# Optimization experiments

Hardware: AMD Instinct MI355X
Metric: run time of the kernel (lower is better)

Reference implementation:

```python
import jax, jax.numpy as jnp
import numpy as np

N_NODES = 100000
N_EDGES = 1200000
IN_DIM = 64
HID = 64
N_GRAPHS = 512
N_CLASSES = 1
LN_EPS = 1e-5
NORM_EPS = 1e-12


def _layer_norm(x, g, b):
    mu = x.mean(-1, keepdims=True)
    var = ((x - mu) ** 2).mean(-1, keepdims=True)
    return (x - mu) * jax.lax.rsqrt(var + LN_EPS) * g + b


def setup_inputs() -> dict:
    key = jax.random.key(0)
    ks = jax.random.split(key, 20)
    h = jax.random.normal(ks[0], (N_NODES, IN_DIM), jnp.float32)
    src = jax.random.randint(ks[1], (N_EDGES,), 0, N_NODES)
    dst = jax.random.randint(ks[2], (N_EDGES,), 0, N_NODES)
    graph_ids = jnp.sort(jax.random.randint(ks[3], (N_NODES,), 0, N_GRAPHS))
    s1 = 1.0 / np.sqrt(IN_DIM)
    s2 = 1.0 / np.sqrt(HID)
    s3 = 1.0 / np.sqrt(2 * HID)
    return {
        "h": h, "src": src, "dst": dst, "graph_ids": graph_ids,
        "W1": jax.random.normal(ks[4], (IN_DIM, HID), jnp.float32) * s1,
        "b1": jnp.zeros((HID,), jnp.float32),
        "W2": jax.random.normal(ks[5], (HID, HID), jnp.float32) * s2,
        "b2": jnp.zeros((HID,), jnp.float32),
        "g1": jnp.ones((HID,), jnp.float32), "be1": jnp.zeros((HID,), jnp.float32),
        "g2": jnp.ones((HID,), jnp.float32), "be2": jnp.zeros((HID,), jnp.float32),
        "g3": jnp.ones((HID,), jnp.float32), "be3": jnp.zeros((HID,), jnp.float32),
        "g4": jnp.ones((HID,), jnp.float32), "be4": jnp.zeros((HID,), jnp.float32),
        "Wc1": jax.random.normal(ks[6], (2 * HID, HID), jnp.float32) * s3,
        "bc1": jnp.zeros((HID,), jnp.float32),
        "Wc2": jax.random.normal(ks[7], (HID, HID), jnp.float32) * s2,
        "bc2": jnp.zeros((HID,), jnp.float32),
        "Wc3": jax.random.normal(ks[8], (HID, N_CLASSES), jnp.float32) * s2,
        "bc3": jnp.zeros((N_CLASSES,), jnp.float32),
    }


def reference(h, src, dst, graph_ids, W1, b1, W2, b2, g1, be1, g2, be2,
              g3, be3, g4, be4, Wc1, bc1, Wc2, bc2, Wc3, bc3):
    N = N_NODES
    ones_e = jnp.ones((src.shape[0],), jnp.float32)
    # DGL GraphConv norm='both': symmetric degree normalization (clamp 0 -> 1)
    deg_out = jnp.clip(jax.ops.segment_sum(ones_e, src, num_segments=N), 1.0)
    deg_in = jnp.clip(jax.ops.segment_sum(ones_e, dst, num_segments=N), 1.0)
    ns = (deg_out ** -0.5)[:, None]
    nd = (deg_in ** -0.5)[:, None]

    def conv(x, W, b):
        msg = (x * ns)[src]                                  # [E, d] gather
        agg = jax.ops.segment_sum(msg, dst, num_segments=N)  # [N, d] scatter-add
        return (agg * nd) @ W + b

    h1 = jax.nn.relu(_layer_norm(conv(h, W1, b1), g1, be1))
    h1 = jax.nn.relu(_layer_norm(conv(h1, W2, b2), g2, be2))

    # per-graph mean / max pooling (dgl.mean_nodes / dgl.max_nodes)
    ssum = jax.ops.segment_sum(h1, graph_ids, num_segments=N_GRAPHS)
    cnt = jnp.clip(jax.ops.segment_sum(jnp.ones((N,), jnp.float32), graph_ids,
                                       num_segments=N_GRAPHS), 1.0)
    hg = ssum / cnt[:, None]
    hg_max = jax.ops.segment_max(h1, graph_ids, num_segments=N_GRAPHS)

    def l2norm(x):  # F.normalize(p=2, dim=1)
        n = jnp.sqrt((x * x).sum(-1, keepdims=True))
        return x / jnp.maximum(n, NORM_EPS)

    hg = jnp.concatenate([l2norm(hg), l2norm(hg_max)], axis=1)  # [G, 2*HID]
    out = jax.nn.relu(_layer_norm(hg @ Wc1 + bc1, g3, be3))
    out = jax.nn.relu(_layer_norm(out @ Wc2 + bc2, g4, be4))
    return out @ Wc3 + bc3
```

## Files before the change

### kernel.cpp

```cpp
#include <hip/hip_runtime.h>
#include <math.h>

#define HID 64
#define LN_EPS 1e-5f
#define NORM_EPS 1e-12f
#define CHUNK 1024
#define CONV_BLOCKS 2048

__device__ __forceinline__ float wave_sum64(float v) {
#pragma unroll
    for (int o = 32; o > 0; o >>= 1) v += __shfl_xor(v, o, 64);
    return v;
}

__global__ __launch_bounds__(256) void count_kernel(const int* __restrict__ src,
                                                    const int* __restrict__ dst,
                                                    int* __restrict__ cnt_out,
                                                    int* __restrict__ cnt_in,
                                                    int E) {
    int e = blockIdx.x * 256 + threadIdx.x;
    if (e >= E) return;
    atomicAdd(&cnt_out[src[e]], 1);
    atomicAdd(&cnt_in[dst[e]], 1);
}

__global__ __launch_bounds__(256) void norm_kernel(int* __restrict__ cnt_out,
                                                   const int* __restrict__ cnt_in,
                                                   float* __restrict__ ns,
                                                   float* __restrict__ nd,
                                                   int N) {
    int n = blockIdx.x * 256 + threadIdx.x;
    if (n >= N) return;
    ns[n] = rsqrtf((float)max(cnt_out[n], 1));
    nd[n] = rsqrtf((float)max(cnt_in[n], 1));
    cnt_out[n] = 0;
}

__global__ __launch_bounds__(256) void scan1_kernel(const int* __restrict__ cnt,
                                                    int* __restrict__ cs,
                                                    int* __restrict__ partials,
                                                    int N) {
    __shared__ int wsum[4];
    int t = threadIdx.x;
    int lane = t & 63, wave = t >> 6;
    int base = blockIdx.x * CHUNK + t * 4;
    int v0 = (base + 0 < N) ? cnt[base + 0] : 0;
    int v1 = (base + 1 < N) ? cnt[base + 1] : 0;
    int v2 = (base + 2 < N) ? cnt[base + 2] : 0;
    int v3 = (base + 3 < N) ? cnt[base + 3] : 0;
    int tsum = v0 + v1 + v2 + v3;
    int x = tsum;
#pragma unroll
    for (int off = 1; off < 64; off <<= 1) {
        int y = __shfl_up(x, off, 64);
        if (lane >= off) x += y;
    }
    if (lane == 63) wsum[wave] = x;
    __syncthreads();
    int waveoff = 0;
    for (int w = 0; w < wave; ++w) waveoff += wsum[w];
    int off0 = waveoff + x - tsum;
    if (base + 0 < N) cs[base + 0] = off0;
    if (base + 1 < N) cs[base + 1] = off0 + v0;
    if (base + 2 < N) cs[base + 2] = off0 + v0 + v1;
    if (base + 3 < N) cs[base + 3] = off0 + v0 + v1 + v2;
    if (t == 255) partials[blockIdx.x] = waveoff + x;
}

__global__ __launch_bounds__(256) void scan2_kernel(int* __restrict__ partials, int nch) {
    __shared__ int wsum[4];
    int t = threadIdx.x;
    int lane = t & 63, wave = t >> 6;
    int base = t * 4;
    int v0 = (base + 0 < nch) ? partials[base + 0] : 0;
    int v1 = (base + 1 < nch) ? partials[base + 1] : 0;
    int v2 = (base + 2 < nch) ? partials[base + 2] : 0;
    int v3 = (base + 3 < nch) ? partials[base + 3] : 0;
    int tsum = v0 + v1 + v2 + v3;
    int x = tsum;
#pragma unroll
    for (int off = 1; off < 64; off <<= 1) {
        int y = __shfl_up(x, off, 64);
        if (lane >= off) x += y;
    }
    if (lane == 63) wsum[wave] = x;
    __syncthreads();
    int waveoff = 0;
    for (int w = 0; w < wave; ++w) waveoff += wsum[w];
    int off0 = waveoff + x - tsum;
    if (base + 0 < nch) partials[base + 0] = off0;
    if (base + 1 < nch) partials[base + 1] = off0 + v0;
    if (base + 2 < nch) partials[base + 2] = off0 + v0 + v1;
    if (base + 3 < nch) partials[base + 3] = off0 + v0 + v1 + v2;
}

__global__ __launch_bounds__(256) void scan3_kernel(int* __restrict__ cs,
                                                    const int* __restrict__ partials,
                                                    int N, int E) {
    int n = blockIdx.x * 256 + threadIdx.x;
    if (n < N) cs[n] += partials[n / CHUNK];
    if (n == 0) cs[N] = E;
}

__global__ __launch_bounds__(256) void fill_kernel(const int* __restrict__ src,
                                                   const int* __restrict__ dst,
                                                   const float* __restrict__ ns,
                                                   const int* __restrict__ cs,
                                                   int* __restrict__ cursor,
                                                   int2* __restrict__ epack,
                                                   int E) {
    int e = blockIdx.x * 256 + threadIdx.x;
    if (e >= E) return;
    int s = src[e];
    int d = dst[e];
    float w = ns[s];
    int p = cs[d] + atomicAdd(&cursor[d], 1);
    epack[p] = make_int2(s, __float_as_int(w));
}

__global__ __launch_bounds__(256) void conv_kernel(const float* __restrict__ x,
                                                   const int2* __restrict__ epack,
                                                   const int* __restrict__ cs,
                                                   const float* __restrict__ nd,
                                                   const float* __restrict__ W,
                                                   const float* __restrict__ b,
                                                   const float* __restrict__ gam,
                                                   const float* __restrict__ bet,
                                                   float* __restrict__ out,
                                                   int N) {
    __shared__ float Ws[HID * HID];
    int tid = threadIdx.x;
    for (int i = tid; i < HID * HID / 4; i += 256) {
        reinterpret_cast<float4*>(Ws)[i] = reinterpret_cast<const float4*>(W)[i];
    }
    __syncthreads();
    int wave = tid >> 6;
    int lane = tid & 63;
    float bl = b[lane], gl = gam[lane], bel = bet[lane];

    for (int n = blockIdx.x * 4 + wave; n < N; n += CONV_BLOCKS * 4) {
        int beg = cs[n], end = cs[n + 1];
        float acc = 0.0f;
        int e = beg;
        for (; e + 4 <= end; e += 4) {
            int2 p0 = epack[e + 0];
            int2 p1 = epack[e + 1];
            int2 p2 = epack[e + 2];
            int2 p3 = epack[e + 3];
            float v0 = x[(size_t)p0.x * HID + lane];
            float v1 = x[(size_t)p1.x * HID + lane];
            float v2 = x[(size_t)p2.x * HID + lane];
            float v3 = x[(size_t)p3.x * HID + lane];
            acc = fmaf(v0, __int_as_float(p0.y), acc);
            acc = fmaf(v1, __int_as_float(p1.y), acc);
            acc = fmaf(v2, __int_as_float(p2.y), acc);
            acc = fmaf(v3, __int_as_float(p3.y), acc);
        }
        for (; e < end; ++e) {
            int2 p = epack[e];
            acc = fmaf(x[(size_t)p.x * HID + lane], __int_as_float(p.y), acc);
        }
        float t = acc * nd[n];

        float y = bl;
#pragma unroll
        for (int k = 0; k < HID; ++k) {
            y = fmaf(__shfl(t, k, 64), Ws[k * HID + lane], y);
        }
        float mu = wave_sum64(y) * (1.0f / HID);
        float d = y - mu;
        float var = wave_sum64(d * d) * (1.0f / HID);
        float o = d * rsqrtf(var + LN_EPS) * gl + bel;
        o = fmaxf(o, 0.0f);
        out[(size_t)n * HID + lane] = o;
    }
}

__global__ __launch_bounds__(256) void pool_kernel(const float* __restrict__ h1,
                                                   const int* __restrict__ gid,
                                                   float* __restrict__ gsum,
                                                   int* __restrict__ gmax,
                                                   float* __restrict__ gcnt,
                                                   int N) {
    int wave = threadIdx.x >> 6;
    int lane = threadIdx.x & 63;
    int strip = blockIdx.x * 4 + wave;
    int base = strip * 64;
    if (base >= N) return;
    int nmax = min(64, N - base);
    int gv = (base + lane < N) ? gid[base + lane] : -1;
    int gcur = __shfl(gv, 0, 64);
    float sum = 0.0f, mx = 0.0f;
    int cnt = 0;
    for (int i = 0; i < nmax; ++i) {
        int g = __shfl(gv, i, 64);
        if (g != gcur) {
            atomicAdd(&gsum[(size_t)gcur * HID + lane], sum);
            atomicMax(&gmax[(size_t)gcur * HID + lane], __float_as_int(mx));
            if (lane == 0) atomicAdd(&gcnt[gcur], (float)cnt);
            sum = 0.0f; mx = 0.0f; cnt = 0; gcur = g;
        }
        float v = h1[((size_t)base + i) * HID + lane];
        sum += v;
        mx = fmaxf(mx, v);
        cnt++;
    }
    atomicAdd(&gsum[(size_t)gcur * HID + lane], sum);
    atomicMax(&gmax[(size_t)gcur * HID + lane], __float_as_int(mx));
    if (lane == 0) atomicAdd(&gcnt[gcur], (float)cnt);
}

__global__ __launch_bounds__(64) void head_kernel(const float* __restrict__ gsum,
                                                  const int* __restrict__ gmax,
                                                  const float* __restrict__ gcnt,
                                                  const float* __restrict__ Wc1,
                                                  const float* __restrict__ bc1,
                                                  const float* __restrict__ g3,
                                                  const float* __restrict__ be3,
                                                  const float* __restrict__ Wc2,
                                                  const float* __restrict__ bc2,
                                                  const float* __restrict__ g4,
                                                  const float* __restrict__ be4,
                                                  const float* __restrict__ Wc3,
                                                  const float* __restrict__ bc3,
                                                  float* __restrict__ out) {
    __shared__ float hg[2 * HID];
    __shared__ float t1[HID];
    int g = blockIdx.x;
    int lane = threadIdx.x;

    float cnt = fmaxf(gcnt[g], 1.0f);
    float mean = gsum[(size_t)g * HID + lane] / cnt;
    float mx = __int_as_float(gmax[(size_t)g * HID + lane]);

    float s1 = sqrtf(wave_sum64(mean * mean));
    float a = mean / fmaxf(s1, NORM_EPS);
    float s2 = sqrtf(wave_sum64(mx * mx));
    float bmx = mx / fmaxf(s2, NORM_EPS);

    hg[lane] = a;
    hg[HID + lane] = bmx;
    __syncthreads();

    float y = bc1[lane];
#pragma unroll 8
    for (int k = 0; k < 2 * HID; ++k) {
        y = fmaf(hg[k], Wc1[k * HID + lane], y);
    }
    float mu = wave_sum64(y) * (1.0f / HID);
    float d = y - mu;
    float var = wave_sum64(d * d) * (1.0f / HID);
    float o = d * rsqrtf(var + LN_EPS) * g3[lane] + be3[lane];
    o = fmaxf(o, 0.0f);
    t1[lane] = o;
    __syncthreads();

    float y2 = bc2[lane];
#pragma unroll 8
    for (int k = 0; k < HID; ++k) {
        y2 = fmaf(t1[k], Wc2[k * HID + lane], y2);
    }
    mu = wave_sum64(y2) * (1.0f / HID);
    d = y2 - mu;
    var = wave_sum64(d * d) * (1.0f / HID);
    o = d * rsqrtf(var + LN_EPS) * g4[lane] + be4[lane];
    o = fmaxf(o, 0.0f);

    float v = o * Wc3[lane];
    v = wave_sum64(v);
    if (lane == 0) out[g] = v + bc3[0];
}

extern "C" void kernel_launch(void* const* d_in, const int* in_sizes, int n_in,
                              void* d_out, int out_size, void* d_ws, size_t ws_size,
                              hipStream_t stream) {
    const float* h   = (const float*)d_in[0];
    const int*   src = (const int*)d_in[1];
    const int*   dst = (const int*)d_in[2];
    const int*   gid = (const int*)d_in[3];
    const float* W1  = (const float*)d_in[4];
    const float* b1  = (const float*)d_in[5];
    const float* W2  = (const float*)d_in[6];
    const float* b2  = (const float*)d_in[7];
    const float* g1  = (const float*)d_in[8];
    const float* be1 = (const float*)d_in[9];
    const float* g2  = (const float*)d_in[10];
    const float* be2 = (const float*)d_in[11];
    const float* g3  = (const float*)d_in[12];
    const float* be3 = (const float*)d_in[13];
    const float* g4  = (const float*)d_in[14];
    const float* be4 = (const float*)d_in[15];
    const float* Wc1 = (const float*)d_in[16];
    const float* bc1 = (const float*)d_in[17];
    const float* Wc2 = (const float*)d_in[18];
    const float* bc2 = (const float*)d_in[19];
    const float* Wc3 = (const float*)d_in[20];
    const float* bc3 = (const float*)d_in[21];
    float* out = (float*)d_out;

    const int N = in_sizes[0] / HID;
    const int E = in_sizes[1];
    const int G = out_size;

    char* ws = (char*)d_ws;
    float* h1     = (float*)ws;
    float* h2     = h1 + (size_t)N * HID;
    int2*  epack  = (int2*)(h2 + (size_t)N * HID);
    float* ns     = (float*)(epack + E);
    float* nd     = ns + N;
    int*   cnt_out= (int*)(nd + N);
    int*   cnt_in = cnt_out + N;
    int*   cs     = cnt_in + N;
    int*   partials = cs + N + 4;
    float* gsum   = (float*)(partials + 1024);
    int*   gmax   = (int*)(gsum + (size_t)G * HID);
    float* gcnt   = (float*)(gmax + (size_t)G * HID);

    const int nch = (N + CHUNK - 1) / CHUNK;

    hipMemsetAsync(cnt_out, 0, sizeof(int) * (size_t)2 * N, stream);
    hipMemsetAsync(gsum, 0, sizeof(float) * (size_t)G * (2 * HID + 1), stream);

    count_kernel<<<(E + 255) / 256, 256, 0, stream>>>(src, dst, cnt_out, cnt_in, E);
    norm_kernel<<<(N + 255) / 256, 256, 0, stream>>>(cnt_out, cnt_in, ns, nd, N);
    scan1_kernel<<<nch, 256, 0, stream>>>(cnt_in, cs, partials, N);
    scan2_kernel<<<1, 256, 0, stream>>>(partials, nch);
    scan3_kernel<<<(N + 255) / 256, 256, 0, stream>>>(cs, partials, N, E);
    fill_kernel<<<(E + 255) / 256, 256, 0, stream>>>(src, dst, ns, cs, cnt_out, epack, E);

    conv_kernel<<<CONV_BLOCKS, 256, 0, stream>>>(h, epack, cs, nd, W1, b1, g1, be1, h1, N);
    conv_kernel<<<CONV_BLOCKS, 256, 0, stream>>>(h1, epack, cs, nd, W2, b2, g2, be2, h2, N);

    int nstrips = (N + 63) / 64;
    pool_kernel<<<(nstrips + 3) / 4, 256, 0, stream>>>(h2, gid, gsum, gmax, gcnt, N);

    head_kernel<<<G, 64, 0, stream>>>(gsum, gmax, gcnt, Wc1, bc1, g3, be3,
                                      Wc2, bc2, g4, be4, Wc3, bc3, out);
}
```

Before: 539.4 us.

## Fuse degree norm into scan, vectorize edge kernels, segment-based pooling

Merges the degree-normalization kernel into the first scan pass and precomputes per-node cursors so the fill step skips reading row offsets. Count and fill kernels each process four edges per thread with vector loads. Pooling now assigns one block per graph, locating its node range by binary search on sorted graph ids, which removes atomics and a memset. The conv kernel gets an occupancy hint and a reduced unroll of the matvec loop, which may change register pressure.

```diff
diff --git a/kernel.cpp b/kernel.cpp
--- a/kernel.cpp
+++ b/kernel.cpp
@@ -13,30 +13,40 @@
     return v;
 }
 
+__device__ __forceinline__ int lower_bound_dev(const int* __restrict__ a, int n, int key) {
+    int lo = 0, hi = n;
+    while (lo < hi) {
+        int mid = (lo + hi) >> 1;
+        if (a[mid] < key) lo = mid + 1; else hi = mid;
+    }
+    return lo;
+}
+
 __global__ __launch_bounds__(256) void count_kernel(const int* __restrict__ src,
                                                     const int* __restrict__ dst,
                                                     int* __restrict__ cnt_out,
                                                     int* __restrict__ cnt_in,
                                                     int E) {
-    int e = blockIdx.x * 256 + threadIdx.x;
-    if (e >= E) return;
-    atomicAdd(&cnt_out[src[e]], 1);
-    atomicAdd(&cnt_in[dst[e]], 1);
-}
-
-__global__ __launch_bounds__(256) void norm_kernel(int* __restrict__ cnt_out,
-                                                   const int* __restrict__ cnt_in,
-                                                   float* __restrict__ ns,
-                                                   float* __restrict__ nd,
-                                                   int N) {
-    int n = blockIdx.x * 256 + threadIdx.x;
-    if (n >= N) return;
-    ns[n] = rsqrtf((float)max(cnt_out[n], 1));
-    nd[n] = rsqrtf((float)max(cnt_in[n], 1));
-    cnt_out[n] = 0;
-}
-
-__global__ __launch_bounds__(256) void scan1_kernel(const int* __restrict__ cnt,
+    int e0 = (blockIdx.x * 256 + threadIdx.x) * 4;
+    if (e0 + 3 < E) {
+        int4 s4 = *reinterpret_cast<const int4*>(src + e0);
+        int4 d4 = *reinterpret_cast<const int4*>(dst + e0);
+        atomicAdd(&cnt_out[s4.x], 1); atomicAdd(&cnt_out[s4.y], 1);
+        atomicAdd(&cnt_out[s4.z], 1); atomicAdd(&cnt_out[s4.w], 1);
+        atomicAdd(&cnt_in[d4.x], 1);  atomicAdd(&cnt_in[d4.y], 1);
+        atomicAdd(&cnt_in[d4.z], 1);  atomicAdd(&cnt_in[d4.w], 1);
+    } else {
+        for (int e = e0; e < E; ++e) {
+            atomicAdd(&cnt_out[src[e]], 1);
+            atomicAdd(&cnt_in[dst[e]], 1);
+        }
+    }
+}
+
+__global__ __launch_bounds__(256) void scan1_kernel(const int* __restrict__ cnt_in,
+                                                    const int* __restrict__ cnt_out,
+                                                    float* __restrict__ ns,
+                                                    float* __restrict__ nd,
                                                     int* __restrict__ cs,
                                                     int* __restrict__ partials,
                                                     int N) {
@@ -44,10 +54,26 @@
     int t = threadIdx.x;
     int lane = t & 63, wave = t >> 6;
     int base = blockIdx.x * CHUNK + t * 4;
-    int v0 = (base + 0 < N) ? cnt[base + 0] : 0;
-    int v1 = (base + 1 < N) ? cnt[base + 1] : 0;
-    int v2 = (base + 2 < N) ? cnt[base + 2] : 0;
-    int v3 = (base + 3 < N) ? cnt[base + 3] : 0;
+    int v0 = (base + 0 < N) ? cnt_in[base + 0] : 0;
+    int v1 = (base + 1 < N) ? cnt_in[base + 1] : 0;
+    int v2 = (base + 2 < N) ? cnt_in[base + 2] : 0;
+    int v3 = (base + 3 < N) ? cnt_in[base + 3] : 0;
+
+    if (base + 3 < N) {
+        int4 co = *reinterpret_cast<const int4*>(cnt_out + base);
+        float4 nsv = make_float4(rsqrtf((float)max(co.x, 1)), rsqrtf((float)max(co.y, 1)),
+                                 rsqrtf((float)max(co.z, 1)), rsqrtf((float)max(co.w, 1)));
+        float4 ndv = make_float4(rsqrtf((float)max(v0, 1)), rsqrtf((float)max(v1, 1)),
+                                 rsqrtf((float)max(v2, 1)), rsqrtf((float)max(v3, 1)));
+        *reinterpret_cast<float4*>(ns + base) = nsv;
+        *reinterpret_cast<float4*>(nd + base) = ndv;
+    } else {
+        for (int i = base; i < N; ++i) {
+            ns[i] = rsqrtf((float)max(cnt_out[i], 1));
+            nd[i] = rsqrtf((float)max(cnt_in[i], 1));
+        }
+    }
+
     int tsum = v0 + v1 + v2 + v3;
     int x = tsum;
 #pragma unroll
@@ -96,40 +122,58 @@
 
 __global__ __launch_bounds__(256) void scan3_kernel(int* __restrict__ cs,
                                                     const int* __restrict__ partials,
+                                                    int* __restrict__ cursor,
                                                     int N, int E) {
     int n = blockIdx.x * 256 + threadIdx.x;
-    if (n < N) cs[n] += partials[n / CHUNK];
+    if (n < N) {
+        int v = cs[n] + partials[n / CHUNK];
+        cs[n] = v;
+        cursor[n] = v;
+    }
     if (n == 0) cs[N] = E;
 }
 
 __global__ __launch_bounds__(256) void fill_kernel(const int* __restrict__ src,
                                                    const int* __restrict__ dst,
                                                    const float* __restrict__ ns,
-                                                   const int* __restrict__ cs,
                                                    int* __restrict__ cursor,
                                                    int2* __restrict__ epack,
                                                    int E) {
-    int e = blockIdx.x * 256 + threadIdx.x;
-    if (e >= E) return;
-    int s = src[e];
-    int d = dst[e];
-    float w = ns[s];
-    int p = cs[d] + atomicAdd(&cursor[d], 1);
-    epack[p] = make_int2(s, __float_as_int(w));
-}
-
-__global__ __launch_bounds__(256) void conv_kernel(const float* __restrict__ x,
-                                                   const int2* __restrict__ epack,
-                                                   const int* __restrict__ cs,
-                                                   const float* __restrict__ nd,
-                                                   const float* __restrict__ W,
-                                                   const float* __restrict__ b,
-                                                   const float* __restrict__ gam,
-                                                   const float* __restrict__ bet,
-                                                   float* __restrict__ out,
-                                                   int N) {
+    int e0 = (blockIdx.x * 256 + threadIdx.x) * 4;
+    if (e0 + 3 < E) {
+        int4 s4 = *reinterpret_cast<const int4*>(src + e0);
+        int4 d4 = *reinterpret_cast<const int4*>(dst + e0);
+        float w0 = ns[s4.x], w1 = ns[s4.y], w2 = ns[s4.z], w3 = ns[s4.w];
+        int p0 = atomicAdd(&cursor[d4.x], 1);
+        int p1 = atomicAdd(&cursor[d4.y], 1);
+        int p2 = atomicAdd(&cursor[d4.z], 1);
+        int p3 = atomicAdd(&cursor[d4.w], 1);
+        epack[p0] = make_int2(s4.x, __float_as_int(w0));
+        epack[p1] = make_int2(s4.y, __float_as_int(w1));
+        epack[p2] = make_int2(s4.z, __float_as_int(w2));
+        epack[p3] = make_int2(s4.w, __float_as_int(w3));
+    } else {
+        for (int e = e0; e < E; ++e) {
+            int s = src[e], d = dst[e];
+            int p = atomicAdd(&cursor[d], 1);
+            epack[p] = make_int2(s, __float_as_int(ns[s]));
+        }
+    }
+}
+
+__global__ __launch_bounds__(256, 8) void conv_kernel(const float* __restrict__ x,
+                                                      const int2* __restrict__ epack,
+                                                      const int* __restrict__ cs,
+                                                      const float* __restrict__ nd,
+                                                      const float* __restrict__ W,
+                                                      const float* __restrict__ b,
+                                                      const float* __restrict__ gam,
+                                                      const float* __restrict__ bet,
+                                                      float* __restrict__ out,
+                                                      int N) {
     __shared__ float Ws[HID * HID];
     int tid = threadIdx.x;
+#pragma unroll
     for (int i = tid; i < HID * HID / 4; i += 256) {
         reinterpret_cast<float4*>(Ws)[i] = reinterpret_cast<const float4*>(W)[i];
     }
@@ -140,6 +184,7 @@
 
     for (int n = blockIdx.x * 4 + wave; n < N; n += CONV_BLOCKS * 4) {
         int beg = cs[n], end = cs[n + 1];
+        float ndv = nd[n];
         float acc = 0.0f;
         int e = beg;
         for (; e + 4 <= end; e += 4) {
@@ -160,10 +205,10 @@
             int2 p = epack[e];
             acc = fmaf(x[(size_t)p.x * HID + lane], __int_as_float(p.y), acc);
         }
-        float t = acc * nd[n];
+        float t = acc * ndv;
 
         float y = bl;
-#pragma unroll
+#pragma unroll 8
         for (int k = 0; k < HID; ++k) {
             y = fmaf(__shfl(t, k, 64), Ws[k * HID + lane], y);
         }
@@ -179,39 +224,39 @@
 __global__ __launch_bounds__(256) void pool_kernel(const float* __restrict__ h1,
                                                    const int* __restrict__ gid,
                                                    float* __restrict__ gsum,
-                                                   int* __restrict__ gmax,
+                                                   float* __restrict__ gmaxf,
                                                    float* __restrict__ gcnt,
                                                    int N) {
-    int wave = threadIdx.x >> 6;
-    int lane = threadIdx.x & 63;
-    int strip = blockIdx.x * 4 + wave;
-    int base = strip * 64;
-    if (base >= N) return;
-    int nmax = min(64, N - base);
-    int gv = (base + lane < N) ? gid[base + lane] : -1;
-    int gcur = __shfl(gv, 0, 64);
+    __shared__ float psum[4][HID];
+    __shared__ float pmax[4][HID];
+    __shared__ int se[2];
+    int g = blockIdx.x;
+    int tid = threadIdx.x;
+    if (tid == 0) se[0] = lower_bound_dev(gid, N, g);
+    if (tid == 64) se[1] = lower_bound_dev(gid, N, g + 1);
+    __syncthreads();
+    int s = se[0], e = se[1];
+    int wave = tid >> 6, lane = tid & 63;
     float sum = 0.0f, mx = 0.0f;
-    int cnt = 0;
-    for (int i = 0; i < nmax; ++i) {
-        int g = __shfl(gv, i, 64);
-        if (g != gcur) {
-            atomicAdd(&gsum[(size_t)gcur * HID + lane], sum);
-            atomicMax(&gmax[(size_t)gcur * HID + lane], __float_as_int(mx));
-            if (lane == 0) atomicAdd(&gcnt[gcur], (float)cnt);
-            sum = 0.0f; mx = 0.0f; cnt = 0; gcur = g;
-        }
-        float v = h1[((size_t)base + i) * HID + lane];
+    for (int r = s + wave; r < e; r += 4) {
+        float v = h1[(size_t)r * HID + lane];
         sum += v;
         mx = fmaxf(mx, v);
-        cnt++;
-    }
-    atomicAdd(&gsum[(size_t)gcur * HID + lane], sum);
-    atomicMax(&gmax[(size_t)gcur * HID + lane], __float_as_int(mx));
-    if (lane == 0) atomicAdd(&gcnt[gcur], (float)cnt);
+    }
+    psum[wave][lane] = sum;
+    pmax[wave][lane] = mx;
+    __syncthreads();
+    if (tid < HID) {
+        float ts = psum[0][tid] + psum[1][tid] + psum[2][tid] + psum[3][tid];
+        float tm = fmaxf(fmaxf(pmax[0][tid], pmax[1][tid]), fmaxf(pmax[2][tid], pmax[3][tid]));
+        gsum[(size_t)g * HID + tid] = ts;
+        gmaxf[(size_t)g * HID + tid] = tm;
+        if (tid == 0) gcnt[g] = (float)(e - s);
+    }
 }
 
 __global__ __launch_bounds__(64) void head_kernel(const float* __restrict__ gsum,
-                                                  const int* __restrict__ gmax,
+                                                  const float* __restrict__ gmaxf,
                                                   const float* __restrict__ gcnt,
                                                   const float* __restrict__ Wc1,
                                                   const float* __restrict__ bc1,
@@ -231,7 +276,7 @@
 
     float cnt = fmaxf(gcnt[g], 1.0f);
     float mean = gsum[(size_t)g * HID + lane] / cnt;
-    float mx = __int_as_float(gmax[(size_t)g * HID + lane]);
+    float mx = gmaxf[(size_t)g * HID + lane];
 
     float s1 = sqrtf(wave_sum64(mean * mean));
     float a = mean / fmaxf(s1, NORM_EPS);
@@ -313,27 +358,25 @@
     int*   cs     = cnt_in + N;
     int*   partials = cs + N + 4;
     float* gsum   = (float*)(partials + 1024);
-    int*   gmax   = (int*)(gsum + (size_t)G * HID);
-    float* gcnt   = (float*)(gmax + (size_t)G * HID);
+    float* gmaxf  = gsum + (size_t)G * HID;
+    float* gcnt   = gmaxf + (size_t)G * HID;
 
     const int nch = (N + CHUNK - 1) / CHUNK;
+    const int E4 = (E + 3) / 4;
 
     hipMemsetAsync(cnt_out, 0, sizeof(int) * (size_t)2 * N, stream);
-    hipMemsetAsync(gsum, 0, sizeof(float) * (size_t)G * (2 * HID + 1), stream);
-
-    count_kernel<<<(E + 255) / 256, 256, 0, stream>>>(src, dst, cnt_out, cnt_in, E);
-    norm_kernel<<<(N + 255) / 256, 256, 0, stream>>>(cnt_out, cnt_in, ns, nd, N);
-    scan1_kernel<<<nch, 256, 0, stream>>>(cnt_in, cs, partials, N);
+
+    count_kernel<<<(E4 + 255) / 256, 256, 0, stream>>>(src, dst, cnt_out, cnt_in, E);
+    scan1_kernel<<<nch, 256, 0, stream>>>(cnt_in, cnt_out, ns, nd, cs, partials, N);
     scan2_kernel<<<1, 256, 0, stream>>>(partials, nch);
-    scan3_kernel<<<(N + 255) / 256, 256, 0, stream>>>(cs, partials, N, E);
-    fill_kernel<<<(E + 255) / 256, 256, 0, stream>>>(src, dst, ns, cs, cnt_out, epack, E);
+    scan3_kernel<<<(N + 255) / 256, 256, 0, stream>>>(cs, partials, cnt_out, N, E);
+    fill_kernel<<<(E4 + 255) / 256, 256, 0, stream>>>(src, dst, ns, cnt_out, epack, E);
 
     conv_kernel<<<CONV_BLOCKS, 256, 0, stream>>>(h, epack, cs, nd, W1, b1, g1, be1, h1, N);
     conv_kernel<<<CONV_BLOCKS, 256, 0, stream>>>(h1, epack, cs, nd, W2, b2, g2, be2, h2, N);
 
-    int nstrips = (N + 63) / 64;
-    pool_kernel<<<(nstrips + 3) / 4, 256, 0, stream>>>(h2, gid, gsum, gmax, gcnt, N);
-
-    head_kernel<<<G, 64, 0, stream>>>(gsum, gmax, gcnt, Wc1, bc1, g3, be3,
+    pool_kernel<<<G, 256, 0, stream>>>(h2, gid, gsum, gmaxf, gcnt, N);
+
+    head_kernel<<<G, 64, 0, stream>>>(gsum, gmaxf, gcnt, Wc1, bc1, g3, be3,
                                       Wc2, bc2, g4, be4, Wc3, bc3, out);
 }
```

Measured after the change: 595.9 us. 1.1x slower.
